# Kernel optimization log

Hardware: AMD Instinct MI355X
Metric: run time of the kernel (lower is better)

## Reference

```python
import jax, jax.numpy as jnp
import numpy as np

D_MODEL = 768
D_STATE = 16
D_CONV = 4
EXPAND = 2
N_LAYERS = 2
HEADDIM = 64
PATCH_DIM = 256
D_INNER = EXPAND * D_MODEL            # 1536
NHEADS = D_INNER // HEADDIM           # 24
CONV_DIM = D_INNER + 2 * D_STATE      # 1568 (x, B, C share the conv)
D_IN_PROJ = 2 * D_INNER + 2 * D_STATE + NHEADS  # 3128


def _mamba2(u, w_in, conv_w, conv_b, dt_bias, A_log, D, norm_w, w_out):
    """Mamba2 block (ngroups=1, rmsnorm=True, non-fused reference path)."""
    b, l, _ = u.shape
    zxbcdt = u @ w_in                                   # (b,l,D_IN_PROJ)
    z = zxbcdt[..., :D_INNER]
    xBC = zxbcdt[..., D_INNER:D_INNER + CONV_DIM]
    dt = jax.nn.softplus(zxbcdt[..., D_INNER + CONV_DIM:] + dt_bias)  # (b,l,H)
    # causal depthwise conv1d over L, then silu
    kernel = conv_w.T[:, None, :]                       # (D_CONV,1,CONV_DIM)
    xBC = jax.lax.conv_general_dilated(
        xBC, kernel, (1,), [(D_CONV - 1, 0)],
        dimension_numbers=('NLC', 'LIO', 'NLC'),
        feature_group_count=CONV_DIM) + conv_b
    xBC = jax.nn.silu(xBC)
    x = xBC[..., :D_INNER].reshape(b, l, NHEADS, HEADDIM)
    B = xBC[..., D_INNER:D_INNER + D_STATE]             # (b,l,N)
    C = xBC[..., D_INNER + D_STATE:]                    # (b,l,N)
    A = -jnp.exp(A_log)                                 # (H,)

    def step(h, inp):
        dt_t, x_t, b_t, c_t = inp                       # (b,H),(b,H,P),(b,N),(b,N)
        dA = jnp.exp(dt_t * A)                          # (b,H)
        h = h * dA[:, :, None, None] + jnp.einsum('bh,bhp,bn->bhpn', dt_t, x_t, b_t)
        y_t = jnp.einsum('bhpn,bn->bhp', h, c_t)
        return h, y_t

    h0 = jnp.zeros((b, NHEADS, HEADDIM, D_STATE), u.dtype)
    _, y = jax.lax.scan(step, h0,
                        (dt.swapaxes(0, 1), x.swapaxes(0, 1),
                         B.swapaxes(0, 1), C.swapaxes(0, 1)))
    y = y.swapaxes(0, 1) + x * D[:, None]               # skip: D per head
    y = y.reshape(b, l, D_INNER)
    # gated RMSNorm: rmsnorm(y * silu(z)) * weight
    g = y * jax.nn.silu(z)
    g = g * jax.lax.rsqrt(jnp.mean(g * g, axis=-1, keepdims=True) + 1e-5)
    y = g * norm_w
    return y @ w_out


def _backbone(patch_embeddings, Wp, bp, in_w, conv_w, conv_b, dt_bias,
              A_log, Dh, norm_w, out_w, bi_w, ls, fin_w):
    x = patch_embeddings @ Wp + bp
    for i in range(N_LAYERS):
        h_f = _mamba2(x, in_w[i, 0], conv_w[i, 0], conv_b[i, 0], dt_bias[i, 0],
                      A_log[i, 0], Dh[i, 0], norm_w[i, 0], out_w[i, 0])
        h_b = jnp.flip(_mamba2(jnp.flip(x, 1), in_w[i, 1], conv_w[i, 1],
                               conv_b[i, 1], dt_bias[i, 1], A_log[i, 1],
                               Dh[i, 1], norm_w[i, 1], out_w[i, 1]), 1)
        m = jnp.concatenate([h_f, h_b], axis=-1) @ bi_w[i]
        x = x + m * ls[i]
    # final RMSNorm with unit offset
    v = jnp.mean(x * x, axis=-1, keepdims=True)
    return x * jax.lax.rsqrt(v + 1e-6) * (1.0 + fin_w)


def setup_inputs() -> dict:
    key = jax.random.key(0)
    ks = jax.random.split(key, 14)
    L2 = (N_LAYERS, 2)
    pe = jax.random.normal(ks[0], (2, 2048, PATCH_DIM), jnp.float32)
    Wp = jax.random.normal(ks[1], (PATCH_DIM, D_MODEL), jnp.float32) * 0.02
    bp = jnp.zeros((D_MODEL,), jnp.float32)
    in_w = jax.random.normal(ks[2], L2 + (D_MODEL, D_IN_PROJ), jnp.float32) * 0.02
    conv_w = jax.random.normal(ks[3], L2 + (CONV_DIM, D_CONV), jnp.float32) * 0.2
    conv_b = jnp.zeros(L2 + (CONV_DIM,), jnp.float32)
    dt_bias = jax.random.uniform(ks[4], L2 + (NHEADS,), jnp.float32, -4.0, -2.0)
    A_log = jnp.log(jax.random.uniform(ks[5], L2 + (NHEADS,), jnp.float32, 1.0, 16.0))
    Dh = jax.random.normal(ks[6], L2 + (NHEADS,), jnp.float32) * 0.1 + 1.0
    norm_w = jnp.ones(L2 + (D_INNER,), jnp.float32)
    out_w = jax.random.normal(ks[7], L2 + (D_INNER, D_MODEL), jnp.float32) * 0.02
    bi_w = jax.random.normal(ks[8], (N_LAYERS, 2 * D_MODEL, D_MODEL), jnp.float32) * 0.02
    ls = jnp.full((N_LAYERS, D_MODEL), 1e-4, jnp.float32)
    fin_w = jnp.zeros((D_MODEL,), jnp.float32)
    return {"patch_embeddings": pe, "Wp": Wp, "bp": bp, "in_w": in_w,
            "conv_w": conv_w, "conv_b": conv_b, "dt_bias": dt_bias,
            "A_log": A_log, "Dh": Dh, "norm_w": norm_w, "out_w": out_w,
            "bi_w": bi_w, "ls": ls, "fin_w": fin_w}


def reference(patch_embeddings, Wp, bp, in_w, conv_w, conv_b, dt_bias,
              A_log, Dh, norm_w, out_w, bi_w, ls, fin_w):
    return _backbone(patch_embeddings, Wp, bp, in_w, conv_w, conv_b, dt_bias,
                     A_log, Dh, norm_w, out_w, bi_w, ls, fin_w)
```

## Files before the change

### kernel.cpp

```cpp
#include <hip/hip_runtime.h>

typedef unsigned short u16;
typedef short s16x8 __attribute__((ext_vector_type(8)));
typedef u16 u16x8 __attribute__((ext_vector_type(8)));
typedef float f32x4 __attribute__((ext_vector_type(4)));

__device__ inline float bf2f(u16 u) {
    union { unsigned int i; float f; } w; w.i = ((unsigned int)u) << 16; return w.f;
}
__device__ inline u16 f2bf(float f) {
    union { float f; unsigned int i; } w; w.f = f;
    unsigned int u = w.i;
    u += 0x7fffu + ((u >> 16) & 1u);
    return (u16)(u >> 16);
}

__global__ __launch_bounds__(256)
void wtransT(const float* __restrict__ src, u16* __restrict__ dst,
             int K, int N, int dstride, int src_z, int dz_hi, int dz_lo)
{
    int z = blockIdx.z;
    src += (size_t)z * src_z;
    dst += (size_t)(z >> 1) * dz_hi + (size_t)(z & 1) * dz_lo;
    __shared__ float t[32][33];
    int kt = blockIdx.y * 32, nt0 = blockIdx.x * 32;
    int lx = threadIdx.x & 31, ly = threadIdx.x >> 5;
#pragma unroll
    for (int i = 0; i < 32; i += 8) {
        int k = kt + ly + i, n = nt0 + lx;
        t[ly + i][lx] = (k < K && n < N) ? src[(size_t)k * N + n] : 0.f;
    }
    __syncthreads();
#pragma unroll
    for (int i = 0; i < 32; i += 8) {
        int n = nt0 + ly + i, k = kt + lx;
        if (n < N && k < K) dst[(size_t)n * dstride + k] = f2bf(t[lx][ly + i]);
    }
}

__global__ void cvtk(const float* __restrict__ src, u16* __restrict__ dst, int n) {
    int i = blockIdx.x * 256 + threadIdx.x;
    if (i < n) dst[i] = f2bf(src[i]);
}

template<int BM, int BN, int EPI>
__global__ __launch_bounds__(256)
void gemmL(const u16* __restrict__ A, const u16* __restrict__ WT,
           int M, int N, int K,
           float* __restrict__ fout, u16* __restrict__ bout,
           const float* __restrict__ bias, const float* __restrict__ lsv,
           int ostride, int ocoloff,
           size_t aZ, size_t wZ, size_t oZ, int ocolZ)
{
    constexpr int MI = BM / 32, NI = BN / 32;
    constexpr int BUF = (BM + BN) * 32;
    constexpr int RA = BM / 64, RB = BN / 64;
    __shared__ u16 lds[2 * BUF];

    {
        int z = blockIdx.z;
        A += (size_t)z * aZ; WT += (size_t)z * wZ;
        bout += (size_t)(z >> 1) * oZ; ocoloff += (z & 1) * ocolZ;
    }

    int mt, nt;
    {
        int nwg = gridDim.x * gridDim.y;
        int f = blockIdx.y * gridDim.x + blockIdx.x;
        int q = nwg >> 3, r = nwg & 7;
        int xcd = f & 7, lo = f >> 3;
        int wid = (xcd < r ? xcd * (q + 1) : r * (q + 1) + (xcd - r) * q) + lo;
        mt = wid % gridDim.y; nt = wid / gridDim.y;
    }

    const int tid  = threadIdx.x;
    const int lane = tid & 63;
    const int wave = tid >> 6;
    const int wm = wave >> 1, wn = wave & 1;
    const int r16 = lane & 15;
    const int ks  = (lane >> 4) * 8;
    const int mb  = mt * BM;
    const int nb  = nt * BN;
    const int wbase = tid & 192;

    f32x4 acc[MI][NI];
#pragma unroll
    for (int mi = 0; mi < MI; mi++)
#pragma unroll
        for (int ni = 0; ni < NI; ni++)
            acc[mi][ni] = (f32x4){0.f, 0.f, 0.f, 0.f};

    auto stage = [&](int buf, int k0) {
        u16* bufA = &lds[buf * BUF];
        u16* bufB = &lds[buf * BUF + BM * 32];
#pragma unroll
        for (int r = 0; r < RA; r++) {
            int c = r * 256 + tid;
            const u16* g = A + (size_t)(mb + (c >> 2)) * K + k0 + (c & 3) * 8;
            __builtin_amdgcn_global_load_lds(
                (const __attribute__((address_space(1))) void*)g,
                (__attribute__((address_space(3))) void*)&bufA[(r * 256 + wbase) * 8],
                16, 0, 0);
        }
#pragma unroll
        for (int r = 0; r < RB; r++) {
            int c = r * 256 + tid;
            const u16* g = WT + (size_t)(nb + (c >> 2)) * K + k0 + (c & 3) * 8;
            __builtin_amdgcn_global_load_lds(
                (const __attribute__((address_space(1))) void*)g,
                (__attribute__((address_space(3))) void*)&bufB[(r * 256 + wbase) * 8],
                16, 0, 0);
        }
    };
    auto compute = [&](int buf) {
        const u16* bufA = &lds[buf * BUF];
        const u16* bufB = &lds[buf * BUF + BM * 32];
        s16x8 af[MI], bfr[NI];
#pragma unroll
        for (int mi = 0; mi < MI; mi++)
            af[mi] = *(const s16x8*)&bufA[(wm * (BM / 2) + mi * 16 + r16) * 32 + ks];
#pragma unroll
        for (int ni = 0; ni < NI; ni++)
            bfr[ni] = *(const s16x8*)&bufB[(wn * (BN / 2) + ni * 16 + r16) * 32 + ks];
#pragma unroll
        for (int mi = 0; mi < MI; mi++)
#pragma unroll
            for (int ni = 0; ni < NI; ni++)
                acc[mi][ni] = __builtin_amdgcn_mfma_f32_16x16x32_bf16(
                    af[mi], bfr[ni], acc[mi][ni], 0, 0, 0);
    };

    const int nt2 = K >> 5;
    stage(0, 0);
    __syncthreads();
    for (int t = 0; t < nt2; t++) {
        if (t + 1 < nt2) stage((t + 1) & 1, (t + 1) << 5);
        compute(t & 1);
        __syncthreads();
    }

#pragma unroll
    for (int mi = 0; mi < MI; mi++) {
        const int rowb = mb + wm * (BM / 2) + mi * 16 + (lane >> 4) * 4;
#pragma unroll
        for (int ni = 0; ni < NI; ni++) {
            int col = nb + wn * (BN / 2) + ni * 16 + r16;
            if (col < N) {
#pragma unroll
                for (int j = 0; j < 4; j++) {
                    int row = rowb + j;
                    float v = acc[mi][ni][j];
                    if (EPI == 0) {
                        v += bias[col];
                        size_t o = (size_t)row * ostride + col;
                        fout[o] = v; bout[o] = f2bf(v);
                    } else if (EPI == 1) {
                        bout[(size_t)row * ostride + ocoloff + col] = f2bf(v);
                    } else {
                        size_t o = (size_t)row * 768 + col;
                        float xv = fout[o] + v * lsv[col];
                        fout[o] = xv; bout[o] = f2bf(xv);
                    }
                }
            }
        }
    }
}

__global__ void dtk(const u16* __restrict__ zxAll, float* __restrict__ dtAll,
                    const float* __restrict__ dtb)
{
    int idx = blockIdx.x * 256 + threadIdx.x;
    if (idx >= 2 * 4096 * 24) return;
    int dir = idx / (4096 * 24);
    int r   = idx % (4096 * 24);
    int row = r / 24, h = r % 24;
    float raw = bf2f(zxAll[(size_t)row * 6256 + dir * 3128 + 3104 + h]) + dtb[dir * 24 + h];
    dtAll[((size_t)dir * 4096 + row) * 24 + h] = raw > 20.f ? raw : log1pf(__expf(raw));
}

__global__ __launch_bounds__(256)
void scan1k(const u16* __restrict__ zxAll, const float* __restrict__ dtAll,
            const float* __restrict__ cw, const float* __restrict__ cb,
            const float* __restrict__ Alog, const float* __restrict__ Dhp,
            u16* __restrict__ yAll, float* __restrict__ states, float* __restrict__ decays)
{
    const int c   = blockIdx.x;
    const int bh  = blockIdx.y;
    const int dir = blockIdx.z;
    const int b = bh / 24, h = bh % 24;
    const float* dtp = dtAll + (size_t)dir * 4096 * 24;
    u16* yp = yAll + dir * 1536;
    const float Av = -__expf(Alog[dir * 24 + h]);
    const float Dv = Dhp[dir * 24 + h];
    const int inst = (dir * 2 + b) * 24 + h;

    const int tid  = threadIdx.x;
    const int lane = tid & 63;
    const int wave = tid >> 6;
    const int r16  = lane & 15;
    const int ks   = (lane >> 4) * 8;

    __shared__ u16 xT[64][72];
    __shared__ u16 Gs[64][72];
    __shared__ u16 Bs[64][40];
    __shared__ u16 Cs[64][40];
    __shared__ u16 SBT[16][72];
    __shared__ float dts[64], cds[64];

    const u16* zxd = zxAll + dir * 3128 + 1536;
    auto growp = [&](int ii) -> const u16* {
        int l = dir ? (2047 - ii) : ii;
        return zxd + ((size_t)b * 2048 + l) * 6256;
    };
    auto rowof = [&](int t) -> size_t {
        int i = c * 64 + t;
        int l = dir ? (2047 - i) : i;
        return (size_t)b * 2048 + l;
    };
    const u16x8 zz = {0,0,0,0,0,0,0,0};

    {
        int tr = tid >> 2, pg = tid & 3;
        int chb = h * 64 + pg * 16;
        int i0 = c * 64 + tr;
        u16x8 tv[4][2];
#pragma unroll
        for (int k = 0; k < 4; k++) {
            int ii = i0 - 3 + k;
            if (ii >= 0) {
                const u16* s = growp(ii) + chb;
                tv[k][0] = *(const u16x8*)s;
                tv[k][1] = *(const u16x8*)(s + 8);
            } else { tv[k][0] = zz; tv[k][1] = zz; }
        }
        const float* cwp = cw + ((size_t)dir * 1568 + chb) * 4;
        const float* cbp = cb + (size_t)dir * 1568 + chb;
#pragma unroll
        for (int j = 0; j < 16; j++) {
            f32x4 wj = *(const f32x4*)(cwp + j * 4);
            float a = cbp[j];
            int hi = j >> 3, lo2 = j & 7;
            a += bf2f(tv[0][hi][lo2]) * wj[0] + bf2f(tv[1][hi][lo2]) * wj[1]
               + bf2f(tv[2][hi][lo2]) * wj[2] + bf2f(tv[3][hi][lo2]) * wj[3];
            a = a / (1.f + __expf(-a));
            xT[pg * 16 + j][tr] = f2bf(a);
        }
    }
    {
        int t = tid & 63, which = tid >> 6;
        if (which < 2) {
            int chb = 1536 + which * 16;
            int i0 = c * 64 + t;
            u16x8 tv[4][2];
#pragma unroll
            for (int k = 0; k < 4; k++) {
                int ii = i0 - 3 + k;
                if (ii >= 0) {
                    const u16* s = growp(ii) + chb;
                    tv[k][0] = *(const u16x8*)s;
                    tv[k][1] = *(const u16x8*)(s + 8);
                } else { tv[k][0] = zz; tv[k][1] = zz; }
            }
            const float* cwp = cw + ((size_t)dir * 1568 + chb) * 4;
            const float* cbp = cb + (size_t)dir * 1568 + chb;
            u16* dst = which ? &Cs[t][0] : &Bs[t][0];
#pragma unroll
            for (int j = 0; j < 16; j++) {
                f32x4 wj = *(const f32x4*)(cwp + j * 4);
                float a = cbp[j];
                int hi = j >> 3, lo2 = j & 7;
                a += bf2f(tv[0][hi][lo2]) * wj[0] + bf2f(tv[1][hi][lo2]) * wj[1]
                   + bf2f(tv[2][hi][lo2]) * wj[2] + bf2f(tv[3][hi][lo2]) * wj[3];
                a = a / (1.f + __expf(-a));
                dst[j] = f2bf(a);
            }
        } else {
            u16* dst = (which == 2) ? &Bs[t][16] : &Cs[t][16];
            *(u16x8*)dst = zz; *(u16x8*)(dst + 8) = zz;
        }
    }
    if (tid < 64) {
        float v = dtp[rowof(tid) * 24 + h];
        dts[tid] = v;
        float s = v;
#pragma unroll
        for (int o = 1; o < 64; o <<= 1) {
            float nvl = __shfl_up(s, o, 64);
            if (lane >= o) s += nvl;
        }
        cds[tid] = s;
    }
    __syncthreads();

    {
        const s16x8 af = *(const s16x8*)&Cs[wave * 16 + r16][ks];
#pragma unroll
        for (int st = 0; st < 4; st++) {
            const s16x8 bfr = *(const s16x8*)&Bs[st * 16 + r16][ks];
            f32x4 a2 = {0.f, 0.f, 0.f, 0.f};
            a2 = __builtin_amdgcn_mfma_f32_16x16x32_bf16(af, bfr, a2, 0, 0, 0);
            int s = st * 16 + (lane & 15);
            int tbase = wave * 16 + (lane >> 4) * 4;
            float cs = cds[s], dtv = dts[s];
#pragma unroll
            for (int j = 0; j < 4; j++) {
                int t = tbase + j;
                float g = 0.f;
                if (s <= t) {
                    g = a2[j] * dtv * __expf(Av * (cds[t] - cs));
                    if (s == t) g += Dv;
                }
                Gs[t][s] = f2bf(g);
            }
        }
    }
    {
        float cdT = cds[63];
        int s = tid & 63;
        float sc = __expf(Av * (cdT - cds[s])) * dts[s];
#pragma unroll
        for (int it = 0; it < 4; it++) {
            int n = (tid >> 6) + it * 4;
            SBT[n][s] = f2bf(sc * bf2f(Bs[s][n]));
        }
    }
    __syncthreads();

    {
#pragma unroll
        for (int pt = 0; pt < 4; pt++) {
            f32x4 a2 = {0.f, 0.f, 0.f, 0.f};
#pragma unroll
            for (int kk = 0; kk < 2; kk++) {
                s16x8 af = *(const s16x8*)&Gs[wave * 16 + r16][kk * 32 + ks];
                s16x8 bfr = *(const s16x8*)&xT[pt * 16 + r16][kk * 32 + ks];
                a2 = __builtin_amdgcn_mfma_f32_16x16x32_bf16(af, bfr, a2, 0, 0, 0);
            }
            int p = pt * 16 + (lane & 15);
            int tbase = wave * 16 + (lane >> 4) * 4;
#pragma unroll
            for (int j = 0; j < 4; j++) {
                size_t row = rowof(tbase + j);
                yp[row * 3072 + h * 64 + p] = f2bf(a2[j]);
            }
        }
    }
    {
        f32x4 a2 = {0.f, 0.f, 0.f, 0.f};
#pragma unroll
        for (int kk = 0; kk < 2; kk++) {
            s16x8 af = *(const s16x8*)&xT[wave * 16 + r16][kk * 32 + ks];
            s16x8 bfr = *(const s16x8*)&SBT[r16][kk * 32 + ks];
            a2 = __builtin_amdgcn_mfma_f32_16x16x32_bf16(af, bfr, a2, 0, 0, 0);
        }
        int n = lane & 15;
        int pbase = wave * 16 + (lane >> 4) * 4;
        float* st = states + ((size_t)inst * 32 + c) * 1024;
#pragma unroll
        for (int j = 0; j < 4; j++) st[(pbase + j) * 16 + n] = a2[j];
        if (tid == 0) decays[inst * 32 + c] = __expf(Av * cds[63]);
    }
}

__global__ __launch_bounds__(256)
void scan2k(float* __restrict__ states, const float* __restrict__ decays)
{
    int inst = blockIdx.x;
    int tid = threadIdx.x;
    float* base = states + (size_t)inst * 32 * 1024 + tid * 4;
    const float* dec = decays + inst * 32;
    f32x4 hreg = {0.f, 0.f, 0.f, 0.f};
    f32x4 L = *(f32x4*)base;
    for (int cc = 0; cc < 32; cc++) {
        f32x4 Lnext;
        if (cc + 1 < 32) Lnext = *(f32x4*)(base + (cc + 1) * 1024);
        *(f32x4*)(base + cc * 1024) = hreg;
        float d = dec[cc];
        hreg = hreg * d + L;
        L = Lnext;
    }
}

__global__ __launch_bounds__(256)
void scan3k(const float* __restrict__ states,
            const u16* __restrict__ zxAll, const float* __restrict__ dtAll,
            const float* __restrict__ cw, const float* __restrict__ cb,
            const float* __restrict__ Alog, u16* __restrict__ yAll)
{
    const int c   = blockIdx.x + 1;
    const int bh  = blockIdx.y;
    const int dir = blockIdx.z;
    const int b = bh / 24, h = bh % 24;
    const float* dtp = dtAll + (size_t)dir * 4096 * 24;
    u16* yp = yAll + dir * 1536;
    const float Av = -__expf(Alog[dir * 24 + h]);
    const int inst = (dir * 2 + b) * 24 + h;
    const int tid = threadIdx.x;

    __shared__ float hs[64][20];
    __shared__ u16 Cs3[64][16];
    __shared__ float ets[64];

    const u16* zxd = zxAll + dir * 3128 + 1536;
    auto growp = [&](int ii) -> const u16* {
        int l = dir ? (2047 - ii) : ii;
        return zxd + ((size_t)b * 2048 + l) * 6256;
    };
    auto rowof = [&](int t) -> size_t {
        int i = c * 64 + t;
        int l = dir ? (2047 - i) : i;
        return (size_t)b * 2048 + l;
    };

    {
        const float* sp = states + ((size_t)inst * 32 + c) * 1024 + tid * 4;
        f32x4 v = *(const f32x4*)sp;
        int e = tid * 4;
        int p = e >> 4, n = e & 15;
        hs[p][n] = v[0]; hs[p][n+1] = v[1]; hs[p][n+2] = v[2]; hs[p][n+3] = v[3];
    }
    if (tid < 64) {
        int i0 = c * 64 + tid;
        u16x8 tv[4][2];
#pragma unroll
        for (int k = 0; k < 4; k++) {
            const u16* s = growp(i0 - 3 + k) + 1552;
            tv[k][0] = *(const u16x8*)s;
            tv[k][1] = *(const u16x8*)(s + 8);
        }
        const float* cwp = cw + ((size_t)dir * 1568 + 1552) * 4;
        const float* cbp = cb + (size_t)dir * 1568 + 1552;
#pragma unroll
        for (int j = 0; j < 16; j++) {
            f32x4 wj = *(const f32x4*)(cwp + j * 4);
            float a = cbp[j];
            int hi = j >> 3, lo2 = j & 7;
            a += bf2f(tv[0][hi][lo2]) * wj[0] + bf2f(tv[1][hi][lo2]) * wj[1]
               + bf2f(tv[2][hi][lo2]) * wj[2] + bf2f(tv[3][hi][lo2]) * wj[3];
            a = a / (1.f + __expf(-a));
            Cs3[tid][j] = f2bf(a);
        }
        float v = dtp[rowof(tid) * 24 + h];
        float s = v;
#pragma unroll
        for (int o = 1; o < 64; o <<= 1) {
            float nvl = __shfl_up(s, o, 64);
            if ((tid & 63) >= o) s += nvl;
        }
        ets[tid] = __expf(Av * s);
    }
    __syncthreads();

    int t = tid >> 2, pg = tid & 3;
    float cv[16];
    float et = ets[t];
#pragma unroll
    for (int n = 0; n < 16; n++) cv[n] = bf2f(Cs3[t][n]) * et;
    size_t row = rowof(t);
    u16* yrow = yp + row * 3072 + h * 64 + pg * 16;
    u16x8 ya = *(u16x8*)yrow;
    u16x8 yb = *(u16x8*)(yrow + 8);
#pragma unroll
    for (int jj = 0; jj < 16; jj++) {
        int p = pg * 16 + jj;
        float acc = 0.f;
#pragma unroll
        for (int q = 0; q < 4; q++) {
            f32x4 hv = *(const f32x4*)&hs[p][q * 4];
            acc += cv[q*4]*hv[0] + cv[q*4+1]*hv[1] + cv[q*4+2]*hv[2] + cv[q*4+3]*hv[3];
        }
        if (jj < 8) ya[jj] = f2bf(bf2f(ya[jj]) + acc);
        else        yb[jj - 8] = f2bf(bf2f(yb[jj - 8]) + acc);
    }
    *(u16x8*)yrow = ya;
    *(u16x8*)(yrow + 8) = yb;
}

__global__ __launch_bounds__(256)
void gatek(const u16* __restrict__ zxAll, u16* __restrict__ yAll,
           const float* __restrict__ nw)
{
    int row = blockIdx.x, dir = blockIdx.y;
    const u16* zx = zxAll + (size_t)row * 6256 + dir * 3128;
    u16* y = yAll + (size_t)row * 3072 + dir * 1536;
    const float* nwp = nw + dir * 1536;
    int tid = threadIdx.x;
    float g[6]; float s = 0.f;
#pragma unroll
    for (int j = 0; j < 6; j++) {
        int c = j * 256 + tid;
        float z  = bf2f(zx[c]);
        float yv = bf2f(y[c]);
        float gv = yv * z / (1.f + __expf(-z));
        g[j] = gv; s += gv * gv;
    }
    __shared__ float red[4];
    for (int o = 32; o; o >>= 1) s += __shfl_down(s, o, 64);
    if ((tid & 63) == 0) red[tid >> 6] = s;
    __syncthreads();
    s = red[0] + red[1] + red[2] + red[3];
    float sc = rsqrtf(s * (1.f / 1536.f) + 1e-5f);
#pragma unroll
    for (int j = 0; j < 6; j++) {
        int c = j * 256 + tid;
        y[c] = f2bf(g[j] * sc * nwp[c]);
    }
}

__global__ __launch_bounds__(256)
void finalk(const float* __restrict__ x, const float* __restrict__ fw, float* __restrict__ out)
{
    int row = blockIdx.x; int tid = threadIdx.x;
    const float* xr = x + (size_t)row * 768;
    float v[3]; float s = 0.f;
#pragma unroll
    for (int j = 0; j < 3; j++) {
        int c = j * 256 + tid;
        v[j] = xr[c]; s += v[j] * v[j];
    }
    __shared__ float red[4];
    for (int o = 32; o; o >>= 1) s += __shfl_down(s, o, 64);
    if ((tid & 63) == 0) red[tid >> 6] = s;
    __syncthreads();
    s = red[0] + red[1] + red[2] + red[3];
    float sc = rsqrtf(s * (1.f / 768.f) + 1e-6f);
#pragma unroll
    for (int j = 0; j < 3; j++) {
        int c = j * 256 + tid;
        out[(size_t)row * 768 + c] = v[j] * sc * (1.f + fw[c]);
    }
}

extern "C" void kernel_launch(void* const* d_in, const int* in_sizes, int n_in,
                              void* d_out, int out_size, void* d_ws, size_t ws_size,
                              hipStream_t stream)
{
    const float* pe      = (const float*)d_in[0];
    const float* Wp      = (const float*)d_in[1];
    const float* bp      = (const float*)d_in[2];
    const float* in_w    = (const float*)d_in[3];
    const float* conv_w  = (const float*)d_in[4];
    const float* conv_b  = (const float*)d_in[5];
    const float* dt_bias = (const float*)d_in[6];
    const float* A_log   = (const float*)d_in[7];
    const float* Dh      = (const float*)d_in[8];
    const float* norm_w  = (const float*)d_in[9];
    const float* out_w   = (const float*)d_in[10];
    const float* bi_w    = (const float*)d_in[11];
    const float* ls      = (const float*)d_in[12];
    const float* fin_w   = (const float*)d_in[13];

    char* wp = (char*)d_ws;
    auto alloc = [&](size_t bytes) {
        char* r = wp; wp += (bytes + 255) & ~(size_t)255; return r;
    };
    u16*   WpT    = (u16*)  alloc((size_t)768 * 256 * 2);
    u16*   inWT   = (u16*)  alloc((size_t)2 * 6272 * 768 * 2);
    u16*   outWB  = (u16*)  alloc((size_t)4 * 1536 * 768 * 2);
    u16*   biWT   = (u16*)  alloc((size_t)4 * 768 * 768 * 2);
    u16*   WcombT = (u16*)  alloc((size_t)2 * 768 * 3072 * 2);
    u16*   peB    = (u16*)  alloc((size_t)4096 * 256 * 2);
    float* x      = (float*)alloc((size_t)4096 * 768 * 4);
    u16*   xb     = (u16*)  alloc((size_t)4096 * 768 * 2);
    u16*   zxAll  = (u16*)  alloc((size_t)4096 * 6256 * 2);
    float* dtAll  = (float*)alloc((size_t)2 * 4096 * 24 * 4);
    u16*   yAll   = (u16*)  alloc((size_t)4096 * 3072 * 2);
    float* states = (float*)alloc((size_t)96 * 32 * 1024 * 4);
    float* decays = (float*)alloc((size_t)96 * 32 * 4);

    wtransT<<<dim3(24, 8, 1), 256, 0, stream>>>(Wp, WpT, 256, 768, 256, 0, 0, 0);
    wtransT<<<dim3(98, 24, 4), 256, 0, stream>>>(in_w, inWT, 768, 3128, 768,
                                                 2402304, 4816896, 2402304);
    wtransT<<<dim3(24, 24, 4), 256, 0, stream>>>(bi_w, biWT, 768, 768, 768,
                                                 589824, 1179648, 589824);
    cvtk<<<(4 * 1536 * 768 + 255) / 256, 256, 0, stream>>>(out_w, outWB, 4 * 1536 * 768);
    cvtk<<<4096, 256, 0, stream>>>(pe, peB, 4096 * 256);

    gemmL<64, 64, 1><<<dim3(24, 12, 4), 256, 0, stream>>>(
        biWT, outWB, 768, 1536, 768, nullptr, WcombT,
        nullptr, nullptr, 3072, 0,
        (size_t)589824, (size_t)1179648, (size_t)768 * 3072, 1536);

    gemmL<64, 64, 0><<<dim3(12, 64, 1), 256, 0, stream>>>(
        peB, WpT, 4096, 768, 256, x, xb, bp, nullptr, 768, 0, 0, 0, 0, 0);

    for (int i = 0; i < 2; i++) {
        gemmL<128, 128, 1><<<dim3(49, 32, 1), 256, 0, stream>>>(
            xb, inWT + (size_t)i * 6272 * 768, 4096, 6256, 768,
            nullptr, zxAll, nullptr, nullptr, 6256, 0, 0, 0, 0, 0);
        dtk<<<(2 * 4096 * 24 + 255) / 256, 256, 0, stream>>>(zxAll, dtAll, dt_bias + i * 48);
        scan1k<<<dim3(32, 48, 2), 256, 0, stream>>>(zxAll, dtAll,
                                                    conv_w + (size_t)i * 2 * 1568 * 4,
                                                    conv_b + (size_t)i * 2 * 1568,
                                                    A_log + i * 48, Dh + i * 48,
                                                    yAll, states, decays);
        scan2k<<<96, 256, 0, stream>>>(states, decays);
        scan3k<<<dim3(31, 48, 2), 256, 0, stream>>>(states, zxAll, dtAll,
                                                    conv_w + (size_t)i * 2 * 1568 * 4,
                                                    conv_b + (size_t)i * 2 * 1568,
                                                    A_log + i * 48, yAll);
        gatek<<<dim3(4096, 2), 256, 0, stream>>>(zxAll, yAll, norm_w + (size_t)i * 2 * 1536);
        gemmL<128, 64, 2><<<dim3(12, 32, 1), 256, 0, stream>>>(
            yAll, WcombT + (size_t)i * 768 * 3072, 4096, 768, 3072,
            x, xb, nullptr, ls + i * 768, 768, 0, 0, 0, 0, 0);
    }

    finalk<<<4096, 256, 0, stream>>>(x, fin_w, (float*)d_out);
}
```

Baseline: 486.4 us.

## Add direct-to-LDS bf16 GEMM with XCD-aware tile mapping for in-projection

Adds a dedicated 128x128 bf16 GEMM for the per-layer input projection. It loads tiles straight into XOR-swizzled LDS with global_load_lds, double-buffers over K in steps of 64, remaps workgroups so each XCD gets contiguous tiles, and raises wave priority around the MFMA block. The goal is to cut register staging and LDS bank conflicts and to improve L2 locality in the largest GEMM. It relies on the padded weight rows (6272) and on M being a multiple of 128, and it drops the generic epilogue paths.

```diff
diff --git a/kernel.cpp b/kernel.cpp
--- a/kernel.cpp
+++ b/kernel.cpp
@@ -41,6 +41,134 @@
 __global__ void cvtk(const float* __restrict__ src, u16* __restrict__ dst, int n) {
     int i = blockIdx.x * 256 + threadIdx.x;
     if (i < n) dst[i] = f2bf(src[i]);
+}
+
+__global__ __launch_bounds__(256, 2)
+void gemm8(const u16* __restrict__ A, const u16* __restrict__ WT,
+           int M, int N, int K,
+           u16* __restrict__ bout, int ostride)
+{
+    __shared__ u16 lds8[2 * 16384];
+
+    int mt, nt;
+    {
+        int nwg = gridDim.x * gridDim.y;
+        int f = blockIdx.y * gridDim.x + blockIdx.x;
+        int q = nwg >> 3, r = nwg & 7;
+        int xcd = f & 7, lo = f >> 3;
+        int wid = (xcd < r ? xcd * (q + 1) : r * (q + 1) + (xcd - r) * q) + lo;
+        mt = wid % gridDim.y; nt = wid / gridDim.y;
+    }
+
+    const int tid  = threadIdx.x;
+    const int lane = tid & 63;
+    const int wave = tid >> 6;
+    const int wm = wave >> 1, wn = wave & 1;
+    const int r16 = lane & 15;
+    const int lg  = lane >> 4;
+    const int mb  = mt * 128;
+    const int nb  = nt * 128;
+    const int wbase = tid & 192;
+
+    f32x4 acc[4][4];
+#pragma unroll
+    for (int mi = 0; mi < 4; mi++)
+#pragma unroll
+        for (int ni = 0; ni < 4; ni++)
+            acc[mi][ni] = (f32x4){0.f, 0.f, 0.f, 0.f};
+
+    auto stage = [&](int buf, int k0) {
+        u16* bA = &lds8[buf * 16384];
+        u16* bB = bA + 8192;
+#pragma unroll
+        for (int r = 0; r < 4; r++) {
+            int e = r * 256 + tid;
+            int row = e >> 3;
+            int cbs = (e & 7) ^ (row & 7);
+            const u16* g = A + (size_t)(mb + row) * K + k0 + cbs * 8;
+            __builtin_amdgcn_global_load_lds(
+                (const __attribute__((address_space(1))) void*)g,
+                (__attribute__((address_space(3))) void*)&bA[(r * 256 + wbase) * 8],
+                16, 0, 0);
+        }
+#pragma unroll
+        for (int r = 0; r < 4; r++) {
+            int e = r * 256 + tid;
+            int row = e >> 3;
+            int cbs = (e & 7) ^ (row & 7);
+            const u16* g = WT + (size_t)(nb + row) * K + k0 + cbs * 8;
+            __builtin_amdgcn_global_load_lds(
+                (const __attribute__((address_space(1))) void*)g,
+                (__attribute__((address_space(3))) void*)&bB[(r * 256 + wbase) * 8],
+                16, 0, 0);
+        }
+    };
+
+    const int ntk = K >> 6;
+    stage(0, 0);
+    stage(1, 64);
+    asm volatile("s_waitcnt vmcnt(8)" ::: "memory");
+    __builtin_amdgcn_sched_barrier(0);
+    __builtin_amdgcn_s_barrier();
+
+    for (int t = 0; t < ntk; t++) {
+        const int buf = t & 1;
+        const u16* bA = &lds8[buf * 16384];
+        const u16* bB = bA + 8192;
+        s16x8 a[4][2], b[4][2];
+#pragma unroll
+        for (int mf = 0; mf < 4; mf++)
+#pragma unroll
+            for (int kk = 0; kk < 2; kk++) {
+                int row = wm * 64 + mf * 16 + r16;
+                int cb = (kk * 4 + lg) ^ (row & 7);
+                a[mf][kk] = *(const s16x8*)&bA[row * 64 + cb * 8];
+            }
+#pragma unroll
+        for (int nf = 0; nf < 4; nf++)
+#pragma unroll
+            for (int kk = 0; kk < 2; kk++) {
+                int row = wn * 64 + nf * 16 + r16;
+                int cb = (kk * 4 + lg) ^ (row & 7);
+                b[nf][kk] = *(const s16x8*)&bB[row * 64 + cb * 8];
+            }
+        asm volatile("s_waitcnt lgkmcnt(0)" ::: "memory");
+        __builtin_amdgcn_sched_barrier(0);
+        __builtin_amdgcn_s_barrier();
+        if (t + 2 < ntk) {
+            stage(buf, (t + 2) << 6);
+            asm volatile("s_waitcnt vmcnt(8)" ::: "memory");
+        } else {
+            asm volatile("s_waitcnt vmcnt(0)" ::: "memory");
+        }
+        __builtin_amdgcn_sched_barrier(0);
+        __builtin_amdgcn_s_barrier();
+        __builtin_amdgcn_s_setprio(1);
+#pragma unroll
+        for (int mf = 0; mf < 4; mf++)
+#pragma unroll
+            for (int nf = 0; nf < 4; nf++) {
+                acc[mf][nf] = __builtin_amdgcn_mfma_f32_16x16x32_bf16(
+                    a[mf][0], b[nf][0], acc[mf][nf], 0, 0, 0);
+                acc[mf][nf] = __builtin_amdgcn_mfma_f32_16x16x32_bf16(
+                    a[mf][1], b[nf][1], acc[mf][nf], 0, 0, 0);
+            }
+        __builtin_amdgcn_s_setprio(0);
+    }
+
+#pragma unroll
+    for (int mf = 0; mf < 4; mf++) {
+        const int rowb = mb + wm * 64 + mf * 16 + lg * 4;
+#pragma unroll
+        for (int nf = 0; nf < 4; nf++) {
+            int col = nb + wn * 64 + nf * 16 + r16;
+            if (col < N) {
+#pragma unroll
+                for (int j = 0; j < 4; j++)
+                    bout[(size_t)(rowb + j) * ostride + col] = f2bf(acc[mf][nf][j]);
+            }
+        }
+    }
 }
 
 template<int BM, int BN, int EPI>
@@ -586,9 +714,8 @@
         peB, WpT, 4096, 768, 256, x, xb, bp, nullptr, 768, 0, 0, 0, 0, 0);
 
     for (int i = 0; i < 2; i++) {
-        gemmL<128, 128, 1><<<dim3(49, 32, 1), 256, 0, stream>>>(
-            xb, inWT + (size_t)i * 6272 * 768, 4096, 6256, 768,
-            nullptr, zxAll, nullptr, nullptr, 6256, 0, 0, 0, 0, 0);
+        gemm8<<<dim3(49, 32, 1), 256, 0, stream>>>(
+            xb, inWT + (size_t)i * 6272 * 768, 4096, 6256, 768, zxAll, 6256);
         dtk<<<(2 * 4096 * 24 + 255) / 256, 256, 0, stream>>>(zxAll, dtAll, dt_bias + i * 48);
         scan1k<<<dim3(32, 48, 2), 256, 0, stream>>>(zxAll, dtAll,
                                                     conv_w + (size_t)i * 2 * 1568 * 4,
```

Result: no change. 489.3 us (+0.6%).
